# Kernel tuning notes

Measured on AMD Instinct MI355X. Metric: run time of the kernel, lower is better.

Reference implementation:

```python
import jax, jax.numpy as jnp
import numpy as np

D_MODEL = 512
N_HEADS = 8
HEAD_DIM = D_MODEL // N_HEADS  # 64
WINDOW = 512
D_FF = 2048
B, L = 4, 8192
EPS = 1e-5


def _layernorm(x, w, b):
    mu = jnp.mean(x, axis=-1, keepdims=True)
    var = jnp.mean(jnp.square(x - mu), axis=-1, keepdims=True)
    return (x - mu) * jax.lax.rsqrt(var + EPS) * w + b


def _rope_cos_sin(seqlen, dim, dtype):
    inv_freq = 1.0 / (10000.0 ** (jnp.arange(0, dim, 2, dtype=jnp.float32) / dim))
    t = jnp.arange(seqlen, dtype=jnp.float32)
    freqs = t[:, None] * inv_freq[None, :]            # [L, dim/2]
    emb = jnp.concatenate([freqs, freqs], axis=-1)     # [L, dim]
    return jnp.cos(emb).astype(dtype), jnp.sin(emb).astype(dtype)


def _apply_rope(x, cos, sin):
    # x: [B,H,L,d]; cos/sin: [L,d]
    d2 = x.shape[-1] // 2
    x1, x2 = x[..., :d2], x[..., d2:]
    rot = jnp.concatenate([-x2, x1], axis=-1)
    return x * cos[None, None] + rot * sin[None, None]


def _window_attn(q, k, v, pad):
    # q,k,v: [B,H,L,d]; pad: [B,L] bool (True = masked key)
    Bn, H, Lq, d = q.shape
    W = WINDOW
    nb = Lq // W
    scale = d ** -0.5
    qb = q.reshape(Bn, H, nb, W, d)
    kz = jnp.pad(k.reshape(Bn, H, nb, W, d), ((0, 0), (0, 0), (1, 0), (0, 0), (0, 0)))
    vz = jnp.pad(v.reshape(Bn, H, nb, W, d), ((0, 0), (0, 0), (1, 0), (0, 0), (0, 0)))
    kwin = jnp.concatenate([kz[:, :, :-1], kz[:, :, 1:]], axis=3)  # [B,H,nb,2W,d]
    vwin = jnp.concatenate([vz[:, :, :-1], vz[:, :, 1:]], axis=3)
    scores = jnp.einsum('bhnqd,bhnkd->bhnqk', qb, kwin) * scale    # [B,H,nb,W,2W]
    ql = jnp.arange(W)[None, :, None]
    kl = jnp.arange(2 * W)[None, None, :]
    nidx = jnp.arange(nb)[:, None, None]
    qg = nidx * W + ql                 # global query idx [nb,W,1]
    kg = nidx * W - W + kl             # global key idx   [nb,1,2W]
    keep = (kg <= qg) & (qg - kg <= W) & (kg >= 0)                 # [nb,W,2W]
    padz = jnp.pad(pad.reshape(Bn, nb, W), ((0, 0), (1, 0), (0, 0)))
    padwin = jnp.concatenate([padz[:, :-1], padz[:, 1:]], axis=2)  # [B,nb,2W]
    mask = keep[None] & ~padwin[:, :, None, :]                     # [B,nb,W,2W]
    scores = jnp.where(mask[:, None], scores, -jnp.inf)
    p = jax.nn.softmax(scores, axis=-1)
    out = jnp.einsum('bhnqk,bhnkd->bhnqd', p, vwin)
    return out.reshape(Bn, H, Lq, d)


def setup_inputs() -> dict:
    key = jax.random.key(0)
    ks = jax.random.split(key, 10)
    s = D_MODEL ** -0.5
    return {
        'x': jax.random.normal(ks[0], (B, L, D_MODEL), dtype=jnp.float32),
        'key_padding_mask': jnp.zeros((B, L), dtype=bool),
        'ln1_w': jnp.ones((D_MODEL,), jnp.float32),
        'ln1_b': jnp.zeros((D_MODEL,), jnp.float32),
        'Wqkv': jax.random.normal(ks[1], (D_MODEL, 3 * D_MODEL), jnp.float32) * s,
        'bqkv': jnp.zeros((3 * D_MODEL,), jnp.float32),
        'Wproj': jax.random.normal(ks[2], (D_MODEL, D_MODEL), jnp.float32) * s,
        'bproj': jnp.zeros((D_MODEL,), jnp.float32),
        'ln2_w': jnp.ones((D_MODEL,), jnp.float32),
        'ln2_b': jnp.zeros((D_MODEL,), jnp.float32),
        'W1': jax.random.normal(ks[3], (D_MODEL, 2 * D_FF), jnp.float32) * s,
        'b1': jnp.zeros((2 * D_FF,), jnp.float32),
        'W2': jax.random.normal(ks[4], (D_FF, D_MODEL), jnp.float32) * (D_FF ** -0.5),
        'b2': jnp.zeros((D_MODEL,), jnp.float32),
    }


def reference(x, key_padding_mask, ln1_w, ln1_b, Wqkv, bqkv, Wproj, bproj,
              ln2_w, ln2_b, W1, b1, W2, b2):
    Bn, Lq, _ = x.shape
    h = _layernorm(x, ln1_w, ln1_b)
    qkv = h @ Wqkv + bqkv
    q, k, v = jnp.split(qkv, 3, axis=-1)
    def shape(t):
        return t.reshape(Bn, Lq, N_HEADS, HEAD_DIM).transpose(0, 2, 1, 3)
    q, k, v = shape(q), shape(k), shape(v)
    cos, sin = _rope_cos_sin(Lq, HEAD_DIM, q.dtype)
    q = _apply_rope(q, cos, sin)
    k = _apply_rope(k, cos, sin)
    attn = _window_attn(q, k, v, key_padding_mask)
    attn = attn.transpose(0, 2, 1, 3).reshape(Bn, Lq, D_MODEL)
    x = x + attn @ Wproj + bproj
    h2 = _layernorm(x, ln2_w, ln2_b)
    g = h2 @ W1 + b1
    a, bgate = jnp.split(g, 2, axis=-1)
    mlp = (jax.nn.silu(a) * bgate) @ W2 + b2
    return x + mlp
```

## Files before the change

kernel.cpp:

```cpp
#include <hip/hip_runtime.h>
#include <math.h>

#define BB 4
#define LL 8192
#define NTOK 32768
#define DM 512
#define NH 8
#define HD 64
#define DFF 2048

typedef __attribute__((ext_vector_type(4))) float f32x4;
typedef __attribute__((ext_vector_type(8))) short s16x8;
typedef __attribute__((ext_vector_type(4))) short s16x4;

static __device__ __forceinline__ float bf2f(short u){
  union { unsigned int i; float f; } c; c.i = ((unsigned int)(unsigned short)u) << 16; return c.f;
}
static __device__ __forceinline__ short f2bf(float x){
  union { float f; unsigned int i; } c; c.f = x;
  unsigned int r = c.i + 0x7fffu + ((c.i >> 16) & 1u);
  return (short)(r >> 16);
}

static __device__ __forceinline__ void gload_lds16(const void* g, void* lds){
  __builtin_amdgcn_global_load_lds(
      (const __attribute__((address_space(1))) unsigned int*)g,
      (__attribute__((address_space(3))) unsigned int*)lds, 16, 0, 0);
}

__global__ void wconv_kernel(const float* __restrict__ in, short* __restrict__ out,
                             int K, int N, int mode){
  __shared__ float t[32][33];
  int c0 = blockIdx.x*32, k0 = blockIdx.y*32;
  int tx = threadIdx.x, ty = threadIdx.y;
#pragma unroll
  for (int j=0;j<4;j++)
    t[ty+8*j][tx] = in[(size_t)(k0+ty+8*j)*N + c0+tx];
  __syncthreads();
#pragma unroll
  for (int j=0;j<4;j++){
    int c = c0+ty+8*j;
    int p = (mode==1) ? ((c<DFF)? (c<<1) : (((c-DFF)<<1)|1)) : c;
    out[(size_t)p*K + k0+tx] = f2bf(t[tx][ty+8*j]);
  }
}

__global__ void rope_table_kernel(float* __restrict__ cosb, float* __restrict__ sinb){
  int i = blockIdx.x*256 + threadIdx.x;
  int l = i >> 5, d = i & 31;
  float inv = powf(10000.f, -(float)d * (1.f/32.f));
  float ang = (float)l * inv;
  cosb[i] = cosf(ang); sinb[i] = sinf(ang);
}

__global__ __launch_bounds__(256) void ln_kernel(const float* __restrict__ x,
      const float* __restrict__ w, const float* __restrict__ bvec,
      short* __restrict__ out){
  int row = blockIdx.x*4 + (threadIdx.x>>6);
  int lane = threadIdx.x & 63;
  const float4* xr = (const float4*)(x + (size_t)row*DM);
  float4 a = xr[lane*2], b = xr[lane*2+1];
  float v[8] = {a.x,a.y,a.z,a.w,b.x,b.y,b.z,b.w};
  float s = 0.f;
#pragma unroll
  for (int j=0;j<8;j++) s += v[j];
#pragma unroll
  for (int m=1;m<64;m<<=1) s += __shfl_xor(s, m);
  float mu = s * (1.f/512.f);
  float q = 0.f;
#pragma unroll
  for (int j=0;j<8;j++){ float d = v[j]-mu; q += d*d; }
#pragma unroll
  for (int m=1;m<64;m<<=1) q += __shfl_xor(q, m);
  float inv = rsqrtf(q*(1.f/512.f) + 1e-5f);
  int d0 = lane*8;
  s16x8 o;
#pragma unroll
  for (int j=0;j<8;j++) o[j] = f2bf((v[j]-mu)*inv*w[d0+j] + bvec[d0+j]);
  *(s16x8*)(out + (size_t)row*DM + d0) = o;
}

__global__ __launch_bounds__(256) void rope_kernel(short* __restrict__ qk,
      const float* __restrict__ cosb, const float* __restrict__ sinb){
  int t = blockIdx.x*256 + threadIdx.x;
  int i = t & 31;
  size_t pos = (size_t)(t >> 5);
  int l = (int)(pos & (LL-1));
  float c = cosb[l*32+i], s = sinb[l*32+i];
  short* base = qk + pos*HD;
  float v1 = bf2f(base[i]), v2 = bf2f(base[i+32]);
  base[i]    = f2bf(v1*c - v2*s);
  base[i+32] = f2bf(v2*c + v1*s);
}

template<int EPI>
__global__ __launch_bounds__(256) void gemm_bt_kernel(
    const short* __restrict__ A, const short* __restrict__ Bt,
    const float* __restrict__ bias, const float* __restrict__ resid,
    void* __restrict__ outp, int M, int N, int K, short* __restrict__ qkvout)
{
  __shared__ short As[128*32];
  __shared__ short Bs[128*32];
  const int tid = threadIdx.x;
  const int w = tid>>6, lane = tid&63;
  const int wr = w>>1, wc = w&1;
  const int l15 = lane&15, l4 = lane>>4;
  const size_t m0 = (size_t)blockIdx.x * 128;
  const size_t n0 = (size_t)blockIdx.y * 128;

  f32x4 acc[4][4] = {};

  for (int k0 = 0; k0 < K; k0 += 32){
    __syncthreads();
#pragma unroll
    for (int i=0;i<2;i++){
      int o = i*4096 + w*1024 + lane*16;
      int row = o>>6, cb = o&63;
      gload_lds16((const char*)A  + ((size_t)(m0+row)*K + k0)*2 + cb,
                  (char*)As + i*4096 + w*1024);
      gload_lds16((const char*)Bt + ((size_t)(n0+row)*K + k0)*2 + cb,
                  (char*)Bs + i*4096 + w*1024);
    }
    __syncthreads();
    s16x8 af[4], bfr[4];
#pragma unroll
    for (int t=0;t<4;t++){
      af[t]  = *(const s16x8*)(As + (wr*64 + t*16 + l15)*32 + l4*8);
      bfr[t] = *(const s16x8*)(Bs + (wc*64 + t*16 + l15)*32 + l4*8);
    }
#pragma unroll
    for (int i=0;i<4;i++)
#pragma unroll
      for (int j=0;j<4;j++)
        acc[i][j] = __builtin_amdgcn_mfma_f32_16x16x32_bf16(af[i], bfr[j], acc[i][j], 0,0,0);
  }

#pragma unroll
  for (int i=0;i<4;i++){
#pragma unroll
    for (int j=0;j<4;j++){
#pragma unroll
      for (int r=0;r<4;r++){
        size_t m = m0 + wr*64 + i*16 + l4*4 + r;
        int n = (int)n0 + wc*64 + j*16 + l15;
        float val = acc[i][j][r];
        if (EPI == 0){
          val += bias[n];
          int which = n>>9, rem = n&511, hh = rem>>6, dd = rem&63;
          size_t bb = m>>13, lp = m&(LL-1);
          qkvout[((((size_t)which*BB + bb)*NH + hh)*LL + lp)*HD + dd] = f2bf(val);
        } else if (EPI == 1){
          val += bias[n] + resid[m*DM + n];
          ((float*)outp)[m*DM + n] = val;
        } else if (EPI == 2){
          int orig = (n&1) ? (DFF + (n>>1)) : (n>>1);
          val += bias[orig];
          float other = __shfl_xor(val, 1);
          if (!(n&1)){
            float sg = val / (1.f + __expf(-val));
            ((short*)outp)[m*(size_t)DFF + (n>>1)] = f2bf(sg * other);
          }
        } else {
          val += bias[n] + resid[m*DM + n];
          ((float*)outp)[m*DM + n] = val;
        }
      }
    }
  }
}

__global__ __launch_bounds__(256) void attn_kernel(
    const short* __restrict__ q, const short* __restrict__ kk,
    const short* __restrict__ vv, const unsigned char* __restrict__ pad,
    short* __restrict__ outp)
{
  const int qt = blockIdx.x;
  const int bh = blockIdx.y;
  const int b = bh >> 3, h = bh & 7;
  const int q0 = qt*64;
  const int tid = threadIdx.x, w = tid>>6, lane = tid&63;
  const int l15 = lane&15, l4 = lane>>4;
  __shared__ short Ks[32*64];
  __shared__ short Vt[64*48];
  __shared__ short Ps[4][16*32];
  __shared__ float mk[32];

  const short* qb = q  + (size_t)bh*LL*HD;
  const short* kb = kk + (size_t)bh*LL*HD;
  const short* vb = vv + (size_t)bh*LL*HD;
  const int qw0 = q0 + w*16;

  s16x8 qf[2];
#pragma unroll
  for (int c=0;c<2;c++)
    qf[c] = *(const s16x8*)(qb + (size_t)(qw0 + l15)*HD + c*32 + l4*8);

  float mrun = -1e30f, ssum = 0.f;
  f32x4 oacc[4] = {};

  const int kc_lo = (q0 >= 512) ? (q0 - 512) : 0;
  const int kc_hi = q0 + 64;

  for (int kc = kc_lo; kc < kc_hi; kc += 32){
    __syncthreads();
    {
      int o = w*1024 + lane*16;
      int row = o>>7, pb = o&127;
      int sb = pb ^ ((row&7)<<4);
      gload_lds16((const char*)kb + ((size_t)(kc+row)*HD)*2 + sb, (char*)Ks + w*1024);
    }
    {
      int krow = tid>>3, d0 = (tid&7)*8;
      s16x8 vload = *(const s16x8*)(vb + (size_t)(kc+krow)*HD + d0);
#pragma unroll
      for (int j=0;j<8;j++) Vt[(d0+j)*48 + krow] = vload[j];
    }
    if (tid < 32) mk[tid] = pad[(size_t)b*LL + kc + tid] ? -1e30f : 0.f;
    __syncthreads();

    bool active = (kc <= qw0+15) && (kc+31 >= qw0-512);
    float p[8];
    if (active){
      f32x4 st[2] = {};
#pragma unroll
      for (int tt=0;tt<2;tt++){
        int key = tt*16 + l15;
        const char* kr = (const char*)Ks + key*128;
        s16x8 kf0 = *(const s16x8*)(kr + ((l4*16)      ^ ((key&7)<<4)));
        s16x8 kf1 = *(const s16x8*)(kr + ((64 + l4*16) ^ ((key&7)<<4)));
        st[tt] = __builtin_amdgcn_mfma_f32_16x16x32_bf16(kf0, qf[0], st[tt],0,0,0);
        st[tt] = __builtin_amdgcn_mfma_f32_16x16x32_bf16(kf1, qf[1], st[tt],0,0,0);
      }
      int qg = qw0 + l15;
      float mx = -1e30f;
      float sv[8];
#pragma unroll
      for (int tt=0;tt<2;tt++)
#pragma unroll
        for (int r=0;r<4;r++){
          int key = kc + tt*16 + l4*4 + r;
          float xv = st[tt][r]*0.125f + mk[tt*16 + l4*4 + r];
          bool ok = (key <= qg) && (key >= qg-512);
          xv = ok ? xv : -1e30f;
          sv[tt*4+r] = xv;
          mx = fmaxf(mx, xv);
        }
      mx = fmaxf(mx, __shfl_xor(mx,16));
      mx = fmaxf(mx, __shfl_xor(mx,32));
      float mnew = fmaxf(mrun, mx);
      float scale = __expf(mrun - mnew);
      float psum = 0.f;
#pragma unroll
      for (int u=0;u<8;u++){ p[u] = __expf(sv[u]-mnew); psum += p[u]; }
      psum += __shfl_xor(psum,16);
      psum += __shfl_xor(psum,32);
      ssum = ssum*scale + psum;
      mrun = mnew;
#pragma unroll
      for (int dt=0;dt<4;dt++) oacc[dt] *= scale;
    }
    __syncthreads();
    if (active){
      short* pw = Ps[w];
#pragma unroll
      for (int tt=0;tt<2;tt++)
#pragma unroll
        for (int r=0;r<4;r++){
          int klog = tt*16 + l4*4 + r;
          pw[l15*32 + (klog ^ ((l15&3)<<3))] = f2bf(p[tt*4+r]);
        }
    }
    __syncthreads();
    if (active){
      const short* pw = Ps[w];
      s16x8 pf = *(const s16x8*)(pw + l15*32 + ((l4*8) ^ ((l15&3)<<3)));
#pragma unroll
      for (int dt=0;dt<4;dt++){
        s16x8 vf = *(const s16x8*)(Vt + (dt*16 + l15)*48 + l4*8);
        oacc[dt] = __builtin_amdgcn_mfma_f32_16x16x32_bf16(vf, pf, oacc[dt],0,0,0);
      }
    }
  }

  float inv = 1.f / ssum;
#pragma unroll
  for (int dt=0;dt<4;dt++){
    s16x4 ov;
#pragma unroll
    for (int r=0;r<4;r++) ov[r] = f2bf(oacc[dt][r]*inv);
    size_t tok = (size_t)b*LL + q0 + w*16 + l15;
    *(s16x4*)(outp + tok*DM + h*HD + dt*16 + l4*4) = ov;
  }
}

extern "C" void kernel_launch(void* const* d_in, const int* in_sizes, int n_in,
                              void* d_out, int out_size, void* d_ws, size_t ws_size,
                              hipStream_t stream) {
  const float* x     = (const float*)d_in[0];
  const unsigned char* mask = (const unsigned char*)d_in[1];
  const float* ln1w  = (const float*)d_in[2];
  const float* ln1b  = (const float*)d_in[3];
  const float* Wqkv  = (const float*)d_in[4];
  const float* bqkv  = (const float*)d_in[5];
  const float* Wproj = (const float*)d_in[6];
  const float* bproj = (const float*)d_in[7];
  const float* ln2w  = (const float*)d_in[8];
  const float* ln2b  = (const float*)d_in[9];
  const float* W1    = (const float*)d_in[10];
  const float* b1    = (const float*)d_in[11];
  const float* W2    = (const float*)d_in[12];
  const float* b2    = (const float*)d_in[13];
  float* out = (float*)d_out;

  char* ws = (char*)d_ws;
  size_t off = 0;
  auto alloc = [&](size_t bytes){ size_t o = off; off += (bytes + 255) & ~(size_t)255; return o; };
  short* wt_qkv = (short*)(ws + alloc((size_t)1536*512*2));
  short* wt_proj= (short*)(ws + alloc((size_t)512*512*2));
  short* wt_w1  = (short*)(ws + alloc((size_t)4096*512*2));
  short* wt_w2  = (short*)(ws + alloc((size_t)512*2048*2));
  float* cosb   = (float*)(ws + alloc((size_t)LL*32*4));
  float* sinb   = (float*)(ws + alloc((size_t)LL*32*4));
  short* hbuf   = (short*)(ws + alloc((size_t)NTOK*DM*2));
  short* qkv    = (short*)(ws + alloc((size_t)3*NTOK*DM*2));
  short* attnb  = (short*)(ws + alloc((size_t)NTOK*DM*2));
  short* mlpb   = qkv;

  dim3 tb32(32,8);
  wconv_kernel<<<dim3(48,16),  tb32, 0, stream>>>(Wqkv,  wt_qkv, 512, 1536, 0);
  wconv_kernel<<<dim3(16,16),  tb32, 0, stream>>>(Wproj, wt_proj, 512, 512, 0);
  wconv_kernel<<<dim3(128,16), tb32, 0, stream>>>(W1,    wt_w1,  512, 4096, 1);
  wconv_kernel<<<dim3(16,64),  tb32, 0, stream>>>(W2,    wt_w2, 2048, 512, 0);
  rope_table_kernel<<<1024, 256, 0, stream>>>(cosb, sinb);

  ln_kernel<<<NTOK/4, 256, 0, stream>>>(x, ln1w, ln1b, hbuf);
  gemm_bt_kernel<0><<<dim3(256,12), 256, 0, stream>>>(hbuf, wt_qkv, bqkv, nullptr,
                                                      nullptr, NTOK, 1536, 512, qkv);
  rope_kernel<<<65536, 256, 0, stream>>>(qkv, cosb, sinb);
  attn_kernel<<<dim3(128,32), 256, 0, stream>>>(qkv, qkv + (size_t)16777216,
                                                qkv + (size_t)33554432, mask, attnb);
  gemm_bt_kernel<1><<<dim3(256,4), 256, 0, stream>>>(attnb, wt_proj, bproj, x,
                                                     out, NTOK, 512, 512, nullptr);
  ln_kernel<<<NTOK/4, 256, 0, stream>>>(out, ln2w, ln2b, hbuf);
  gemm_bt_kernel<2><<<dim3(256,32), 256, 0, stream>>>(hbuf, wt_w1, b1, nullptr,
                                                      mlpb, NTOK, 4096, 512, nullptr);
  gemm_bt_kernel<3><<<dim3(256,4), 256, 0, stream>>>(mlpb, wt_w2, b2, out,
                                                     out, NTOK, 512, 2048, nullptr);
  (void)in_sizes; (void)n_in; (void)out_size; (void)ws_size;
}
```

Before: 900.9 us.

## Replace GEMM with 256x256 tiled, double-buffered, swizzled-LDS pipelined kernel

Replaces the 128x128 single-buffered GEMM with a 256x256 tile, 512-thread kernel that uses BK=64, double-buffered LDS with XOR swizzling, and prefetches two k-tiles ahead. MFMA issue is interleaved with LDS reads and global loads, using explicit waitcnt, barriers and setprio. A grouped block-index swizzle is added for L2 locality. Larger tiles raise arithmetic intensity and overlap memory with compute, but use far more registers and LDS (128KB), which limits occupancy, and the small N=512 GEMMs launch only 256 blocks.

Result: faster. 818.9 us (-9.1%).

```diff
diff --git a/kernel.cpp b/kernel.cpp
--- a/kernel.cpp
+++ b/kernel.cpp
@@ -94,55 +94,163 @@
 }
 
 template<int EPI>
-__global__ __launch_bounds__(256) void gemm_bt_kernel(
+__global__ __launch_bounds__(512,2) void gemm256_kernel(
     const short* __restrict__ A, const short* __restrict__ Bt,
     const float* __restrict__ bias, const float* __restrict__ resid,
-    void* __restrict__ outp, int M, int N, int K, short* __restrict__ qkvout)
+    void* __restrict__ outp, int K, short* __restrict__ qkvout)
 {
-  __shared__ short As[128*32];
-  __shared__ short Bs[128*32];
+  __shared__ short As[2][16384];
+  __shared__ short Bs[2][16384];
   const int tid = threadIdx.x;
   const int w = tid>>6, lane = tid&63;
-  const int wr = w>>1, wc = w&1;
+  const int wm = w>>2, wn = w&3;
   const int l15 = lane&15, l4 = lane>>4;
-  const size_t m0 = (size_t)blockIdx.x * 128;
-  const size_t n0 = (size_t)blockIdx.y * 128;
-
-  f32x4 acc[4][4] = {};
-
-  for (int k0 = 0; k0 < K; k0 += 32){
-    __syncthreads();
+
+  const int nwg = gridDim.x;
+  const int bid = blockIdx.x;
+  const int bsw = (bid&7)*(nwg>>3) + (bid>>3);
+  const int mblk = bsw & 127;
+  const int nblk = bsw >> 7;
+  const size_t m0 = (size_t)mblk << 8;
+  const size_t n0 = (size_t)nblk << 8;
+  const int nt = K >> 6;
+
+  auto stage2 = [&](const short* __restrict__ g, int row0g, int kt, short* unitbase){
 #pragma unroll
     for (int i=0;i<2;i++){
-      int o = i*4096 + w*1024 + lane*16;
-      int row = o>>6, cb = o&63;
-      gload_lds16((const char*)A  + ((size_t)(m0+row)*K + k0)*2 + cb,
-                  (char*)As + i*4096 + w*1024);
-      gload_lds16((const char*)Bt + ((size_t)(n0+row)*K + k0)*2 + cb,
-                  (char*)Bs + i*4096 + w*1024);
-    }
-    __syncthreads();
-    s16x8 af[4], bfr[4];
-#pragma unroll
-    for (int t=0;t<4;t++){
-      af[t]  = *(const s16x8*)(As + (wr*64 + t*16 + l15)*32 + l4*8);
-      bfr[t] = *(const s16x8*)(Bs + (wc*64 + t*16 + l15)*32 + l4*8);
-    }
-#pragma unroll
-    for (int i=0;i<4;i++)
-#pragma unroll
-      for (int j=0;j<4;j++)
-        acc[i][j] = __builtin_amdgcn_mfma_f32_16x16x32_bf16(af[i], bfr[j], acc[i][j], 0,0,0);
-  }
-
-#pragma unroll
-  for (int i=0;i<4;i++){
+      int c = w*128 + i*64 + lane;
+      int rin = c>>3, s = c&7;
+      int grow = row0g + rin;
+      gload_lds16((const char*)g + (((size_t)grow*K + (kt<<6))<<1) + ((s ^ (grow&7))<<4),
+                  (char*)unitbase + w*2048 + i*1024);
+    }
+  };
+
+  f32x4 acc[8][4] = {};
+  s16x8 aR[4][2], bR[4][2];
+
+  stage2(Bt, (int)n0,       0, &Bs[0][0]);
+  stage2(Bt, (int)n0 + 128, 0, &Bs[0][8192]);
+  stage2(A,  (int)m0,       0, &As[0][0]);
+  stage2(A,  (int)m0 + 128, 0, &As[0][8192]);
+  if (nt > 1){
+    stage2(Bt, (int)n0,       1, &Bs[1][0]);
+    stage2(Bt, (int)n0 + 128, 1, &Bs[1][8192]);
+    stage2(A,  (int)m0,       1, &As[1][0]);
+    stage2(A,  (int)m0 + 128, 1, &As[1][8192]);
+    asm volatile("s_waitcnt vmcnt(8)" ::: "memory");
+  } else {
+    asm volatile("s_waitcnt vmcnt(0)" ::: "memory");
+  }
+  __builtin_amdgcn_s_barrier();
+
+  for (int t=0; t<nt; ++t){
+    const char* Ab = (const char*)As[t&1];
+    const char* Bb = (const char*)Bs[t&1];
+    const bool st = (t+2) < nt;
+
+#pragma unroll
+    for (int mf=0;mf<4;mf++)
+#pragma unroll
+      for (int kh=0;kh<2;kh++){
+        int row = wm*128 + mf*16 + l15;
+        aR[mf][kh] = *(const s16x8*)(Ab + row*128 + (((kh<<6) + (l4<<4)) ^ ((row&7)<<4)));
+      }
+#pragma unroll
+    for (int nf=0;nf<2;nf++)
+#pragma unroll
+      for (int kh=0;kh<2;kh++){
+        int row = wn*64 + nf*16 + l15;
+        bR[nf][kh] = *(const s16x8*)(Bb + row*128 + (((kh<<6) + (l4<<4)) ^ ((row&7)<<4)));
+      }
+    asm volatile("s_waitcnt lgkmcnt(8)" ::: "memory");
+    __builtin_amdgcn_s_barrier();
+    asm volatile("s_waitcnt lgkmcnt(0)" ::: "memory");
+    __builtin_amdgcn_sched_barrier(0);
+    __builtin_amdgcn_s_setprio(1);
+#pragma unroll
+    for (int mf=0;mf<4;mf++)
+#pragma unroll
+      for (int nf=0;nf<2;nf++)
+#pragma unroll
+        for (int kh=0;kh<2;kh++)
+          acc[mf][nf] = __builtin_amdgcn_mfma_f32_16x16x32_bf16(aR[mf][kh], bR[nf][kh], acc[mf][nf],0,0,0);
+    __builtin_amdgcn_s_setprio(0);
+    __builtin_amdgcn_s_barrier();
+
+#pragma unroll
+    for (int nf=2;nf<4;nf++)
+#pragma unroll
+      for (int kh=0;kh<2;kh++){
+        int row = wn*64 + nf*16 + l15;
+        bR[nf][kh] = *(const s16x8*)(Bb + row*128 + (((kh<<6) + (l4<<4)) ^ ((row&7)<<4)));
+      }
+    __builtin_amdgcn_s_barrier();
+    asm volatile("s_waitcnt lgkmcnt(0)" ::: "memory");
+    __builtin_amdgcn_sched_barrier(0);
+    __builtin_amdgcn_s_setprio(1);
+#pragma unroll
+    for (int mf=0;mf<4;mf++)
+#pragma unroll
+      for (int nf=2;nf<4;nf++)
+#pragma unroll
+        for (int kh=0;kh<2;kh++)
+          acc[mf][nf] = __builtin_amdgcn_mfma_f32_16x16x32_bf16(aR[mf][kh], bR[nf][kh], acc[mf][nf],0,0,0);
+    __builtin_amdgcn_s_setprio(0);
+    __builtin_amdgcn_s_barrier();
+
+#pragma unroll
+    for (int mf=0;mf<4;mf++)
+#pragma unroll
+      for (int kh=0;kh<2;kh++){
+        int row = wm*128 + 64 + mf*16 + l15;
+        aR[mf][kh] = *(const s16x8*)(Ab + row*128 + (((kh<<6) + (l4<<4)) ^ ((row&7)<<4)));
+      }
+    if (st){
+      stage2(Bt, (int)n0,       t+2, &Bs[t&1][0]);
+      stage2(Bt, (int)n0 + 128, t+2, &Bs[t&1][8192]);
+    }
+    __builtin_amdgcn_s_barrier();
+    asm volatile("s_waitcnt lgkmcnt(0)" ::: "memory");
+    __builtin_amdgcn_sched_barrier(0);
+    __builtin_amdgcn_s_setprio(1);
+#pragma unroll
+    for (int mf=0;mf<4;mf++)
+#pragma unroll
+      for (int nf=0;nf<2;nf++)
+#pragma unroll
+        for (int kh=0;kh<2;kh++)
+          acc[mf+4][nf] = __builtin_amdgcn_mfma_f32_16x16x32_bf16(aR[mf][kh], bR[nf][kh], acc[mf+4][nf],0,0,0);
+    __builtin_amdgcn_s_setprio(0);
+    __builtin_amdgcn_s_barrier();
+
+    if (st){
+      stage2(A, (int)m0,       t+2, &As[t&1][0]);
+      stage2(A, (int)m0 + 128, t+2, &As[t&1][8192]);
+    }
+    __builtin_amdgcn_s_barrier();
+    __builtin_amdgcn_s_setprio(1);
+#pragma unroll
+    for (int mf=0;mf<4;mf++)
+#pragma unroll
+      for (int nf=2;nf<4;nf++)
+#pragma unroll
+        for (int kh=0;kh<2;kh++)
+          acc[mf+4][nf] = __builtin_amdgcn_mfma_f32_16x16x32_bf16(aR[mf][kh], bR[nf][kh], acc[mf+4][nf],0,0,0);
+    __builtin_amdgcn_s_setprio(0);
+    if (st)               { asm volatile("s_waitcnt vmcnt(8)" ::: "memory"); }
+    else if (t+1 < nt)    { asm volatile("s_waitcnt vmcnt(0)" ::: "memory"); }
+    __builtin_amdgcn_s_barrier();
+  }
+
+#pragma unroll
+  for (int i=0;i<8;i++){
 #pragma unroll
     for (int j=0;j<4;j++){
 #pragma unroll
       for (int r=0;r<4;r++){
-        size_t m = m0 + wr*64 + i*16 + l4*4 + r;
-        int n = (int)n0 + wc*64 + j*16 + l15;
+        size_t m = m0 + wm*128 + i*16 + l4*4 + r;
+        int n = (int)n0 + wn*64 + j*16 + l15;
         float val = acc[i][j][r];
         if (EPI == 0){
           val += bias[n];
@@ -334,17 +442,17 @@
   rope_table_kernel<<<1024, 256, 0, stream>>>(cosb, sinb);
 
   ln_kernel<<<NTOK/4, 256, 0, stream>>>(x, ln1w, ln1b, hbuf);
-  gemm_bt_kernel<0><<<dim3(256,12), 256, 0, stream>>>(hbuf, wt_qkv, bqkv, nullptr,
-                                                      nullptr, NTOK, 1536, 512, qkv);
+  gemm256_kernel<0><<<768, 512, 0, stream>>>(hbuf, wt_qkv, bqkv, nullptr,
+                                             nullptr, 512, qkv);
   rope_kernel<<<65536, 256, 0, stream>>>(qkv, cosb, sinb);
   attn_kernel<<<dim3(128,32), 256, 0, stream>>>(qkv, qkv + (size_t)16777216,
                                                 qkv + (size_t)33554432, mask, attnb);
-  gemm_bt_kernel<1><<<dim3(256,4), 256, 0, stream>>>(attnb, wt_proj, bproj, x,
-                                                     out, NTOK, 512, 512, nullptr);
+  gemm256_kernel<1><<<256, 512, 0, stream>>>(attnb, wt_proj, bproj, x,
+                                             out, 512, nullptr);
   ln_kernel<<<NTOK/4, 256, 0, stream>>>(out, ln2w, ln2b, hbuf);
-  gemm_bt_kernel<2><<<dim3(256,32), 256, 0, stream>>>(hbuf, wt_w1, b1, nullptr,
-                                                      mlpb, NTOK, 4096, 512, nullptr);
-  gemm_bt_kernel<3><<<dim3(256,4), 256, 0, stream>>>(mlpb, wt_w2, b2, out,
-                                                     out, NTOK, 512, 2048, nullptr);
+  gemm256_kernel<2><<<2048, 512, 0, stream>>>(hbuf, wt_w1, b1, nullptr,
+                                              mlpb, 512, nullptr);
+  gemm256_kernel<3><<<256, 512, 0, stream>>>(mlpb, wt_w2, b2, out,
+                                             out, 2048, nullptr);
   (void)in_sizes; (void)n_in; (void)out_size; (void)ws_size;
 }
```
